# Kernel optimization log

Measured on AMD Instinct MI355X. Metric: run time of the kernel, lower is better.

## Reference

```python
import jax, jax.numpy as jnp
import numpy as np
import math

# Product of P Lorentz hyperboloids, each of dim D (time coord first), curvature c (K = 1/c).
N, P, D = 30000, 4, 64   # nodes, sub-manifolds, dim per sub-manifold
E = 480000               # edges (COO sparse adjacency)
C_IN, C_OUT = 1.0, 1.0
MIN_NORM = 1e-15
EPS = 1e-7
MAX_NORM = 1000.0


def _arcosh(x):
    return jnp.log(x + jnp.sqrt(jnp.maximum(x * x - 1.0, MIN_NORM)))


def proj(x, K):
    # project onto hyperboloid: recompute time coordinate from space coords
    y = x[..., 1:]
    t = jnp.sqrt(jnp.maximum(K + jnp.sum(y * y, -1, keepdims=True), EPS))
    return jnp.concatenate([t, y], -1)


def proj_tan0(u):
    # tangent space at origin: zero out the time coordinate
    return jnp.concatenate([jnp.zeros_like(u[..., :1]), u[..., 1:]], -1)


def proj_tan(u, x, K):
    ux = jnp.sum(x[..., 1:] * u[..., 1:], -1, keepdims=True)
    t = ux / jnp.maximum(x[..., :1], MIN_NORM)
    return jnp.concatenate([t, u[..., 1:]], -1)


def expmap0(u, K):
    sqrtK = K ** 0.5
    sp = u[..., 1:]
    n = jnp.maximum(jnp.linalg.norm(sp, axis=-1, keepdims=True), MIN_NORM)
    theta = n / sqrtK
    time = sqrtK * jnp.cosh(theta)
    space = sqrtK * jnp.sinh(theta) * sp / n
    return proj(jnp.concatenate([time, space], -1), K)


def logmap0(x, K):
    sqrtK = K ** 0.5
    sp = x[..., 1:]
    n = jnp.maximum(jnp.linalg.norm(sp, axis=-1, keepdims=True), MIN_NORM)
    theta = jnp.maximum(x[..., :1] / sqrtK, 1.0 + EPS)
    space = sqrtK * _arcosh(theta) * sp / n
    return jnp.concatenate([jnp.zeros_like(theta), space], -1)


def mink_dot(x, y):
    return jnp.sum(x[..., 1:] * y[..., 1:], -1, keepdims=True) - x[..., :1] * y[..., :1]


def expmap(u, x, K):
    sqrtK = K ** 0.5
    normu = jnp.minimum(jnp.sqrt(jnp.maximum(mink_dot(u, u), EPS)), MAX_NORM)
    theta = jnp.maximum(normu / sqrtK, MIN_NORM)
    return proj(jnp.cosh(theta) * x + jnp.sinh(theta) * u / theta, K)


def ptransp0(x, u, K):
    # parallel transport of tangent u at origin to point x
    sqrtK = K ** 0.5
    x0 = x[..., :1]
    y = x[..., 1:]
    yn = jnp.maximum(jnp.linalg.norm(y, axis=-1, keepdims=True), MIN_NORM)
    yu = y / yn
    v = jnp.concatenate([-yn, (sqrtK - x0) * yu], -1)
    alpha = jnp.sum(yu * u[..., 1:], -1, keepdims=True) / sqrtK
    return proj_tan(u - alpha * v, x, K)


def mobius_add(x, y, K):
    return expmap(ptransp0(x, logmap0(y, K), K), x, K)


def setup_inputs() -> dict:
    key = jax.random.key(0)
    k1, k2, k3, k4, k5 = jax.random.split(key, 5)
    K = 1.0 / C_IN
    # valid points on the product manifold: expmap0 of random tangent vectors
    t = 0.1 * jax.random.normal(k1, (N, P, D), dtype=jnp.float32)
    x = proj(expmap0(proj_tan0(t), K), K).reshape(N, P * D)
    adj_row = jax.random.randint(k2, (E,), 0, N)
    adj_col = jax.random.randint(k3, (E,), 0, N)
    # roughly degree-normalized positive adjacency weights
    adj_val = jax.random.uniform(k4, (E,), dtype=jnp.float32) / 16.0
    fan = P * D
    gain = math.sqrt(2.0) * math.sqrt(2.0 / (fan + fan))  # xavier_uniform(gain=sqrt(2)) scale
    weight = gain * jax.random.normal(k5, (fan, fan), dtype=jnp.float32)
    bias = jnp.full((fan,), 1e-4, dtype=jnp.float32)  # init.constant_(bias, 0.0001)
    return {"x": x, "adj_val": adj_val, "weight": weight, "bias": bias,
            "adj_row": adj_row, "adj_col": adj_col}


def reference(x, adj_val, weight, bias, adj_row, adj_col):
    K = 1.0 / C_IN
    Ko = 1.0 / C_OUT
    xs = x.reshape(N, P, D)

    # ---- ProLinear: mobius_matvec + hyperbolic bias add ----
    u = logmap0(xs, K).reshape(N, P * D)          # tangent at origin, concat across sub-manifolds
    mu = (u @ weight.T).reshape(N, P, D)          # [N, P*D] @ [P*D, P*D]^T
    h = proj(expmap0(proj_tan0(mu), K), K)
    b = bias.reshape(1, P, D)
    hyp_bias = proj(expmap0(proj_tan0(b), K), K)
    h = proj(mobius_add(h, hyp_bias, K), K)

    # ---- ProAgg: logmap0 -> spmm -> clamp -> expmap0 ----
    xt = logmap0(h, K).reshape(N, P * D)
    msgs = adj_val[:, None] * xt[adj_col]          # [E, P*D] gather
    support = jax.ops.segment_sum(msgs, adj_row, num_segments=N)
    support = jnp.minimum(support, MAX_NORM).reshape(N, P, D)
    h = proj(expmap0(proj_tan0(support), K), K)

    # ---- ProAct: logmap0 (c_in) -> clamped relu -> expmap0 (c_out) ----
    t = logmap0(h, K)
    t = jnp.minimum(jax.nn.relu(t), MAX_NORM)
    out = expmap0(proj_tan0(t), Ko)
    return out.reshape(N, P * D)
```

## Files before the change

### kernel.cpp

```cpp
#include <hip/hip_runtime.h>
#include <hip/hip_bf16.h>

#define MIN_NORM 1e-15f
#define EPS 1e-7f
#define MAX_NORM 1000.0f

#define NN 30000
#define PP 4
#define DD 64
#define EE 480000

typedef __attribute__((ext_vector_type(8))) short short8v;
typedef __attribute__((ext_vector_type(4))) float float4v;

__device__ inline float frcp(float x) { return __builtin_amdgcn_rcpf(x); }
__device__ inline float bf2f(unsigned short u) { return __uint_as_float(((unsigned)u) << 16); }
__device__ inline unsigned short f2bf(float f) {
    unsigned u = __float_as_uint(f);
    return (unsigned short)((u + 0x7fffu + ((u >> 16) & 1u)) >> 16);
}

__device__ inline float wsum(float v) {
#pragma unroll
    for (int off = 32; off >= 1; off >>= 1) v += __shfl_xor(v, off, 64);
    return v;
}
__device__ inline float expmap0_proj_pt(float v, int lane) {
    float sp = (lane == 0) ? 0.f : v;
    float n2 = wsum(sp * sp);
    float n = fmaxf(sqrtf(n2), MIN_NORM);
    float ep = __expf(n), em = frcp(ep);
    float s = 0.5f * (ep - em) * frcp(n);
    float time = sqrtf(fmaxf(1.f + s * s * n2, EPS));
    return (lane == 0) ? time : s * sp;
}
__device__ inline float logmap0_pt(float x, int lane) {
    float sp = (lane == 0) ? 0.f : x;
    float n2 = wsum(sp * sp);
    float n = fmaxf(sqrtf(n2), MIN_NORM);
    float x0 = __shfl(x, 0, 64);
    float th = fmaxf(x0, 1.f + EPS);
    float ac = __logf(th + sqrtf(fmaxf(th * th - 1.f, MIN_NORM)));
    return (lane == 0) ? 0.f : (ac * sp * frcp(n));
}
__device__ inline float gsum16(float v) {
#pragma unroll
    for (int off = 8; off >= 1; off >>= 1) v += __shfl_xor(v, off, 64);
    return v;
}
__device__ inline void gsum16x4(float& a, float& b, float& c, float& d) {
#pragma unroll
    for (int off = 8; off >= 1; off >>= 1) {
        a += __shfl_xor(a, off, 64);
        b += __shfl_xor(b, off, 64);
        c += __shfl_xor(c, off, 64);
        d += __shfl_xor(d, off, 64);
    }
}

__global__ void prep_kernel(const float* __restrict__ w,
                            unsigned short* __restrict__ bhi,
                            unsigned short* __restrict__ blo) {
    int tt = blockIdx.x * 256 + threadIdx.x;
    int lane = tt & 63;
    int ks = (tt >> 6) & 7;
    int nt = tt >> 9;
    int col = nt * 16 + (lane & 15);
    int kb = ks * 32 + (lane >> 4) * 8;
#pragma unroll
    for (int e = 0; e < 8; e++) {
        float v = w[col * 256 + kb + e];
        unsigned short h = f2bf(v);
        bhi[tt * 8 + e] = h;
        blo[tt * 8 + e] = f2bf(v - bf2f(h));
    }
}

#define GR 16
#define UPITCH 264
__global__ __launch_bounds__(256) void fused_front_hist_kernel(const float* __restrict__ x,
                                                               const unsigned short* __restrict__ bhi,
                                                               const unsigned short* __restrict__ blo,
                                                               const float* __restrict__ bias,
                                                               unsigned short* __restrict__ xt,
                                                               const int* __restrict__ adj_row,
                                                               int* __restrict__ counts) {
    __shared__ __align__(16) char smem[17952];
    unsigned short* uh = (unsigned short*)smem;
    unsigned short* ul = (unsigned short*)(smem + 8448);
    float* uspL = (float*)(smem + 16896);
    float* u2L  = (float*)(smem + 17920);

    int tid = threadIdx.x;
    int lane = tid & 63;
    int wv = tid >> 6;
    int row0 = blockIdx.x * GR;

    atomicAdd(&counts[adj_row[blockIdx.x * 256 + tid]], 1);

    {
        float b = bias[wv * 64 + lane];
        float y = expmap0_proj_pt(b, lane);
        float usp = logmap0_pt(y, lane);
        float U2 = wsum(usp * usp);
        uspL[wv * 64 + lane] = usp;
        if (lane == 0) u2L[wv] = U2;
    }

    int r = tid >> 4, l = tid & 15;
    {
        const float4* xr = (const float4*)(x + (size_t)(row0 + r) * 256);
        float4 a[4];
#pragma unroll
        for (int p = 0; p < 4; p++) a[p] = xr[p * 16 + l];
        float s0, s1, s2, s3;
        {
            float m0 = (l == 0) ? 0.f : a[0].x;
            float m1 = (l == 0) ? 0.f : a[1].x;
            float m2 = (l == 0) ? 0.f : a[2].x;
            float m3 = (l == 0) ? 0.f : a[3].x;
            s0 = m0 * m0 + a[0].y * a[0].y + a[0].z * a[0].z + a[0].w * a[0].w;
            s1 = m1 * m1 + a[1].y * a[1].y + a[1].z * a[1].z + a[1].w * a[1].w;
            s2 = m2 * m2 + a[2].y * a[2].y + a[2].z * a[2].z + a[2].w * a[2].w;
            s3 = m3 * m3 + a[3].y * a[3].y + a[3].z * a[3].z + a[3].w * a[3].w;
        }
        gsum16x4(s0, s1, s2, s3);
        float n2a[4] = {s0, s1, s2, s3};
#pragma unroll
        for (int p = 0; p < 4; p++) {
            float n2 = n2a[p];
            float n = fmaxf(sqrtf(n2), MIN_NORM);
            float th = fmaxf(sqrtf(1.f + n2), 1.f + EPS);
            float ac = __logf(th + sqrtf(fmaxf(th * th - 1.f, MIN_NORM)));
            float sc = ac * frcp(n);
            float ux0 = (l == 0) ? 0.f : sc * a[p].x;
            float uy = sc * a[p].y, uz = sc * a[p].z, uw = sc * a[p].w;
            unsigned short hx = f2bf(ux0), hy = f2bf(uy), hz = f2bf(uz), hw = f2bf(uw);
            ushort4 hv = {hx, hy, hz, hw};
            ushort4 lv = {f2bf(ux0 - bf2f(hx)), f2bf(uy - bf2f(hy)),
                          f2bf(uz - bf2f(hz)), f2bf(uw - bf2f(hw))};
            *(ushort4*)(uh + r * UPITCH + p * 64 + 4 * l) = hv;
            *(ushort4*)(ul + r * UPITCH + p * 64 + 4 * l) = lv;
        }
    }
    __syncthreads();

    float4v acc[4];
#pragma unroll
    for (int j = 0; j < 4; j++) acc[j] = (float4v){0.f, 0.f, 0.f, 0.f};
    int abyte = (lane & 15) * (UPITCH * 2) + (lane >> 4) * 16;
#pragma unroll
    for (int ks = 0; ks < 8; ks++) {
        short8v Ah = *(const short8v*)(smem + abyte + ks * 64);
        short8v Al = *(const short8v*)(smem + 8448 + abyte + ks * 64);
#pragma unroll
        for (int j = 0; j < 4; j++) {
            size_t chunk = ((size_t)((wv * 4 + j) * 8 + ks) * 64 + lane) * 8;
            short8v Bh = *(const short8v*)(bhi + chunk);
            short8v Bl = *(const short8v*)(blo + chunk);
            acc[j] = __builtin_amdgcn_mfma_f32_16x16x32_bf16(Ah, Bh, acc[j], 0, 0, 0);
            acc[j] = __builtin_amdgcn_mfma_f32_16x16x32_bf16(Al, Bh, acc[j], 0, 0, 0);
            acc[j] = __builtin_amdgcn_mfma_f32_16x16x32_bf16(Ah, Bl, acc[j], 0, 0, 0);
        }
    }

    int lp = lane & 15, hi = lane >> 4;
    float uf[4];
#pragma unroll
    for (int j = 0; j < 4; j++) uf[j] = uspL[wv * 64 + j * 16 + lp];
    if (lp == 0) {
        acc[0][0] = 0.f; acc[0][1] = 0.f; acc[0][2] = 0.f; acc[0][3] = 0.f;
    }
    float n2v[4], duv[4];
#pragma unroll
    for (int reg = 0; reg < 4; reg++) {
        float pn = 0.f, pd = 0.f;
#pragma unroll
        for (int j = 0; j < 4; j++) {
            pn = fmaf(acc[j][reg], acc[j][reg], pn);
            pd = fmaf(acc[j][reg], uf[j], pd);
        }
        n2v[reg] = pn; duv[reg] = pd;
    }
#pragma unroll
    for (int off = 1; off < 16; off <<= 1) {
#pragma unroll
        for (int reg = 0; reg < 4; reg++) {
            n2v[reg] += __shfl_xor(n2v[reg], off, 64);
            duv[reg] += __shfl_xor(duv[reg], off, 64);
        }
    }
    float U2 = u2L[wv];

    float A[4], Bc[4];
#pragma unroll
    for (int reg = 0; reg < 4; reg++) {
        float n2 = n2v[reg], duu = duv[reg];
        float n = fmaxf(sqrtf(n2), MIN_NORM);
        float epv = __expf(n), emv = frcp(epv);
        float sv = 0.5f * (epv - emv) * frcp(n);
        float hs2 = sv * sv * n2;
        float h0 = sqrtf(fmaxf(1.f + hs2, EPS));
        float yn = fmaxf(sv * n, MIN_NORM);
        float dhu = sv * duu;
        float alpha = dhu * frcp(yn);
        float g = alpha * (1.f - h0);
        float ux = dhu - g * yn;
        float t = ux * frcp(fmaxf(h0, MIN_NORM));
        float w2 = U2 - 2.f * g * alpha + g * g;
        float md = w2 - t * t;
        float normu = fminf(sqrtf(fmaxf(md, EPS)), MAX_NORM);
        float theta = fmaxf(normu, MIN_NORM);
        float ep2 = __expf(theta), em2 = frcp(ep2);
        float ch = 0.5f * (ep2 + em2);
        float shot = 0.5f * (ep2 - em2) * frcp(theta);
        float rn2 = ch * ch * hs2 + 2.f * ch * shot * ux + shot * shot * w2;
        float rtime = sqrtf(fmaxf(1.f + rn2, EPS));
        float th2 = fmaxf(rtime, 1.f + EPS);
        float ac2 = __logf(th2 + sqrtf(fmaxf(th2 * th2 - 1.f, MIN_NORM)));
        float rn = fmaxf(sqrtf(rn2), MIN_NORM);
        float K = ac2 * frcp(rn);
        A[reg] = K * sv * (ch - shot * g * frcp(yn));
        Bc[reg] = K * shot;
    }

    unsigned short* xbase = xt + (size_t)(row0 + hi * 4) * 256 + wv * 64 + lp;
#pragma unroll
    for (int reg = 0; reg < 4; reg++) {
#pragma unroll
        for (int j = 0; j < 4; j++) {
            float o = fmaf(A[reg], acc[j][reg], Bc[reg] * uf[j]);
            xbase[reg * 256 + j * 16] = f2bf(o);
        }
    }
}

#define SCH 32
__global__ __launch_bounds__(1024) void scan_kernel(const int* __restrict__ counts,
                                                    int* __restrict__ starts, int n) {
    int tid = threadIdx.x, lane = tid & 63, wv = tid >> 6;
    int i0 = tid * SCH;
    int c[SCH];
    const int4* c4 = (const int4*)(counts + i0);
#pragma unroll
    for (int q = 0; q < 8; q++) {
        int4 v = c4[q];
        c[4 * q] = v.x; c[4 * q + 1] = v.y; c[4 * q + 2] = v.z; c[4 * q + 3] = v.w;
    }
    int s = 0;
#pragma unroll
    for (int j = 0; j < SCH; j++) s += c[j];
    int incl = s;
#pragma unroll
    for (int off = 1; off < 64; off <<= 1) {
        int t = __shfl_up(incl, off, 64);
        if (lane >= off) incl += t;
    }
    __shared__ int wtot[16];
    if (lane == 63) wtot[wv] = incl;
    __syncthreads();
    if (wv == 0 && lane < 16) {
        int v = wtot[lane];
        int sc = v;
#pragma unroll
        for (int off = 1; off < 16; off <<= 1) {
            int t = __shfl_up(sc, off, 64);
            if (lane >= off) sc += t;
        }
        wtot[lane] = sc - v;
    }
    __syncthreads();
    int run = incl - s + wtot[wv];
#pragma unroll
    for (int j = 0; j < SCH; j++) {
        int idx = i0 + j;
        if (idx < n) starts[idx] = run;
        run += c[j];
    }
    if (tid == 1023) starts[n] = run;
}

__global__ void scatter_kernel(const int* __restrict__ row, const int* __restrict__ col,
                               const float* __restrict__ val, const int* __restrict__ starts,
                               int* __restrict__ cursor, int2* __restrict__ ep, int E) {
    int e = blockIdx.x * 256 + threadIdx.x;
    if (e < E) {
        int r = row[e];
        int pos = starts[r] + atomicAdd(&cursor[r], 1);
        ep[pos] = make_int2(col[e], __float_as_int(val[e]));
    }
}

__global__ __launch_bounds__(256) void spmm_final_kernel(const unsigned short* __restrict__ xt,
                                                         const int2* __restrict__ ep,
                                                         const int* __restrict__ starts,
                                                         float4* __restrict__ out4) {
    int w = threadIdx.x >> 6;
    int lane = threadIdx.x & 63;
    int r = blockIdx.x * 4 + w;
    int s = starts[r], e = starts[r + 1];

    float4 acc = {0.f, 0.f, 0.f, 0.f};
    for (int i = s; i < e; i += 8) {
        int cs[8]; float vs[8];
#pragma unroll
        for (int u = 0; u < 8; u++) {
            int idx = i + u;
            bool ok = idx < e;
            int2 pe = ep[ok ? idx : s];
            cs[u] = pe.x;
            vs[u] = ok ? __int_as_float(pe.y) : 0.f;
        }
        ushort4 av[8];
#pragma unroll
        for (int u = 0; u < 8; u++)
            av[u] = *(const ushort4*)(xt + ((size_t)cs[u] << 8) + (lane << 2));
#pragma unroll
        for (int u = 0; u < 8; u++) {
            acc.x = fmaf(vs[u], bf2f(av[u].x), acc.x);
            acc.y = fmaf(vs[u], bf2f(av[u].y), acc.y);
            acc.z = fmaf(vs[u], bf2f(av[u].z), acc.z);
            acc.w = fmaf(vs[u], bf2f(av[u].w), acc.w);
        }
    }

    acc.x = fminf(acc.x, MAX_NORM); acc.y = fminf(acc.y, MAX_NORM);
    acc.z = fminf(acc.z, MAX_NORM); acc.w = fminf(acc.w, MAX_NORM);

    bool leader = ((lane & 15) == 0);
    float4 sp = acc;
    if (leader) sp.x = 0.f;
    float n2 = gsum16(sp.x * sp.x + sp.y * sp.y + sp.z * sp.z + sp.w * sp.w);
    float n = fmaxf(sqrtf(n2), MIN_NORM);
    float ep1 = __expf(n), em1 = frcp(ep1);
    float s1 = 0.5f * (ep1 - em1) * frcp(n);
    float hs2 = s1 * s1 * n2;
    float time = sqrtf(fmaxf(1.f + hs2, EPS));
    float th = fmaxf(time, 1.f + EPS);
    float ac = __logf(th + sqrtf(fmaxf(th * th - 1.f, MIN_NORM)));
    float hn = fmaxf(s1 * n, MIN_NORM);
    float sc = ac * s1 * frcp(hn);
    float4 t;
    t.x = leader ? 0.f : sc * sp.x;
    t.y = sc * sp.y;
    t.z = sc * sp.z;
    t.w = sc * sp.w;
    t.x = fminf(fmaxf(t.x, 0.f), MAX_NORM);
    t.y = fminf(fmaxf(t.y, 0.f), MAX_NORM);
    t.z = fminf(fmaxf(t.z, 0.f), MAX_NORM);
    t.w = fminf(fmaxf(t.w, 0.f), MAX_NORM);
    float t2 = gsum16(t.x * t.x + t.y * t.y + t.z * t.z + t.w * t.w);
    float nt = fmaxf(sqrtf(t2), MIN_NORM);
    float ep3 = __expf(nt), em3 = frcp(ep3);
    float s3 = 0.5f * (ep3 - em3) * frcp(nt);
    float time3 = sqrtf(fmaxf(1.f + s3 * s3 * t2, EPS));
    float4 o;
    o.x = leader ? time3 : s3 * t.x;
    o.y = s3 * t.y;
    o.z = s3 * t.z;
    o.w = s3 * t.w;

    out4[(size_t)r * 64 + lane] = o;
}

extern "C" void kernel_launch(void* const* d_in, const int* in_sizes, int n_in,
                              void* d_out, int out_size, void* d_ws, size_t ws_size,
                              hipStream_t stream) {
    const float* x       = (const float*)d_in[0];
    const float* adj_val = (const float*)d_in[1];
    const float* weight  = (const float*)d_in[2];
    const float* bias    = (const float*)d_in[3];
    const int*   adj_row = (const int*)d_in[4];
    const int*   adj_col = (const int*)d_in[5];

    const int N = NN, E = EE;

    unsigned short* B   = (unsigned short*)d_ws;
    unsigned short* Whi = B + (size_t)N * 256;
    unsigned short* Wlo = Whi + 65536;
    int* counts  = (int*)(Wlo + 65536);
    int* cursor  = counts + N;
    int* starts  = cursor + N;
    int2* ep     = (int2*)(starts + N + 2);

    hipMemsetAsync(counts, 0, 2 * N * sizeof(int), stream);
    prep_kernel<<<32, 256, 0, stream>>>(weight, Whi, Wlo);
    fused_front_hist_kernel<<<N / GR, 256, 0, stream>>>(x, Whi, Wlo, bias, B,
                                                        adj_row, counts);
    scan_kernel<<<1, 1024, 0, stream>>>(counts, starts, N);
    scatter_kernel<<<(E + 255) / 256, 256, 0, stream>>>(adj_row, adj_col, adj_val,
                                                        starts, cursor, ep, E);
    spmm_final_kernel<<<N / 4, 256, 0, stream>>>(B, ep, starts, (float4*)d_out);
}
```

Measured before the change: 149.9 us.

## Hoist bias transform, dedupe per-row scalar math, packed bf16 cvt, dynamic row queue in spmm

The bias expmap/logmap computation moves out of every front block into one extra block of the prep kernel, and its results are read from global memory. Per-row scalar math in the front kernel (arcosh scale, A/B coefficients) is now computed once per lane and broadcast with shuffles instead of being repeated in every lane. The bf16 hi/lo split uses the packed v_cvt_pk_bf16_f32 instruction. The spmm kernel switches to a persistent grid of 2048 blocks in which each wavefront pulls rows from an atomic counter, to balance uneven row degrees. This adds atomic traffic and reads ep entries past a row's end, with column indices clamped and values zeroed.

```diff
diff --git a/kernel.cpp b/kernel.cpp
--- a/kernel.cpp
+++ b/kernel.cpp
@@ -18,6 +18,11 @@
 __device__ inline unsigned short f2bf(float f) {
     unsigned u = __float_as_uint(f);
     return (unsigned short)((u + 0x7fffu + ((u >> 16) & 1u)) >> 16);
+}
+__device__ inline unsigned pk_bf16(float a, float b) {
+    unsigned r;
+    asm("v_cvt_pk_bf16_f32 %0, %1, %2" : "=v"(r) : "v"(a), "v"(b));
+    return r;
 }
 
 __device__ inline float wsum(float v) {
@@ -60,7 +65,21 @@
 
 __global__ void prep_kernel(const float* __restrict__ w,
                             unsigned short* __restrict__ bhi,
-                            unsigned short* __restrict__ blo) {
+                            unsigned short* __restrict__ blo,
+                            const float* __restrict__ bias,
+                            float* __restrict__ uspG,
+                            float* __restrict__ u2G) {
+    if (blockIdx.x == 32) {
+        int lane = threadIdx.x & 63;
+        int wv = threadIdx.x >> 6;
+        float b = bias[wv * 64 + lane];
+        float y = expmap0_proj_pt(b, lane);
+        float usp = logmap0_pt(y, lane);
+        float U2 = wsum(usp * usp);
+        uspG[wv * 64 + lane] = usp;
+        if (lane == 0) u2G[wv] = U2;
+        return;
+    }
     int tt = blockIdx.x * 256 + threadIdx.x;
     int lane = tt & 63;
     int ks = (tt >> 6) & 7;
@@ -81,15 +100,14 @@
 __global__ __launch_bounds__(256) void fused_front_hist_kernel(const float* __restrict__ x,
                                                                const unsigned short* __restrict__ bhi,
                                                                const unsigned short* __restrict__ blo,
-                                                               const float* __restrict__ bias,
+                                                               const float* __restrict__ uspG,
+                                                               const float* __restrict__ u2G,
                                                                unsigned short* __restrict__ xt,
                                                                const int* __restrict__ adj_row,
                                                                int* __restrict__ counts) {
-    __shared__ __align__(16) char smem[17952];
+    __shared__ __align__(16) char smem[16896];
     unsigned short* uh = (unsigned short*)smem;
     unsigned short* ul = (unsigned short*)(smem + 8448);
-    float* uspL = (float*)(smem + 16896);
-    float* u2L  = (float*)(smem + 17920);
 
     int tid = threadIdx.x;
     int lane = tid & 63;
@@ -97,15 +115,6 @@
     int row0 = blockIdx.x * GR;
 
     atomicAdd(&counts[adj_row[blockIdx.x * 256 + tid]], 1);
-
-    {
-        float b = bias[wv * 64 + lane];
-        float y = expmap0_proj_pt(b, lane);
-        float usp = logmap0_pt(y, lane);
-        float U2 = wsum(usp * usp);
-        uspL[wv * 64 + lane] = usp;
-        if (lane == 0) u2L[wv] = U2;
-    }
 
     int r = tid >> 4, l = tid & 15;
     {
@@ -125,22 +134,28 @@
             s3 = m3 * m3 + a[3].y * a[3].y + a[3].z * a[3].z + a[3].w * a[3].w;
         }
         gsum16x4(s0, s1, s2, s3);
-        float n2a[4] = {s0, s1, s2, s3};
+        float n2m = (l & 2) ? ((l & 1) ? s3 : s2) : ((l & 1) ? s1 : s0);
+        float scm;
+        {
+            float n = fmaxf(sqrtf(n2m), MIN_NORM);
+            float th = fmaxf(sqrtf(1.f + n2m), 1.f + EPS);
+            float ac = __logf(th + sqrtf(fmaxf(th * th - 1.f, MIN_NORM)));
+            scm = ac * frcp(n);
+        }
+        int gbase = lane & 48;
 #pragma unroll
         for (int p = 0; p < 4; p++) {
-            float n2 = n2a[p];
-            float n = fmaxf(sqrtf(n2), MIN_NORM);
-            float th = fmaxf(sqrtf(1.f + n2), 1.f + EPS);
-            float ac = __logf(th + sqrtf(fmaxf(th * th - 1.f, MIN_NORM)));
-            float sc = ac * frcp(n);
-            float ux0 = (l == 0) ? 0.f : sc * a[p].x;
-            float uy = sc * a[p].y, uz = sc * a[p].z, uw = sc * a[p].w;
-            unsigned short hx = f2bf(ux0), hy = f2bf(uy), hz = f2bf(uz), hw = f2bf(uw);
-            ushort4 hv = {hx, hy, hz, hw};
-            ushort4 lv = {f2bf(ux0 - bf2f(hx)), f2bf(uy - bf2f(hy)),
-                          f2bf(uz - bf2f(hz)), f2bf(uw - bf2f(hw))};
-            *(ushort4*)(uh + r * UPITCH + p * 64 + 4 * l) = hv;
-            *(ushort4*)(ul + r * UPITCH + p * 64 + 4 * l) = lv;
+            float sc = __shfl(scm, gbase + p, 64);
+            float u0 = (l == 0) ? 0.f : sc * a[p].x;
+            float u1 = sc * a[p].y, u2 = sc * a[p].z, u3 = sc * a[p].w;
+            unsigned h01 = pk_bf16(u0, u1), h23 = pk_bf16(u2, u3);
+            float r0 = u0 - __uint_as_float(h01 << 16);
+            float r1 = u1 - __uint_as_float(h01 & 0xFFFF0000u);
+            float r2 = u2 - __uint_as_float(h23 << 16);
+            float r3 = u3 - __uint_as_float(h23 & 0xFFFF0000u);
+            unsigned lo01 = pk_bf16(r0, r1), lo23 = pk_bf16(r2, r3);
+            *(uint2*)(uh + r * UPITCH + p * 64 + 4 * l) = make_uint2(h01, h23);
+            *(uint2*)(ul + r * UPITCH + p * 64 + 4 * l) = make_uint2(lo01, lo23);
         }
     }
     __syncthreads();
@@ -167,7 +182,8 @@
     int lp = lane & 15, hi = lane >> 4;
     float uf[4];
 #pragma unroll
-    for (int j = 0; j < 4; j++) uf[j] = uspL[wv * 64 + j * 16 + lp];
+    for (int j = 0; j < 4; j++) uf[j] = uspG[wv * 64 + j * 16 + lp];
+    float U2 = u2G[wv];
     if (lp == 0) {
         acc[0][0] = 0.f; acc[0][1] = 0.f; acc[0][2] = 0.f; acc[0][3] = 0.f;
     }
@@ -190,12 +206,12 @@
             duv[reg] += __shfl_xor(duv[reg], off, 64);
         }
     }
-    float U2 = u2L[wv];
-
-    float A[4], Bc[4];
-#pragma unroll
-    for (int reg = 0; reg < 4; reg++) {
-        float n2 = n2v[reg], duu = duv[reg];
+
+    float Am, Bm;
+    {
+        int sel = lp & 3;
+        float n2 = (sel & 2) ? ((sel & 1) ? n2v[3] : n2v[2]) : ((sel & 1) ? n2v[1] : n2v[0]);
+        float duu = (sel & 2) ? ((sel & 1) ? duv[3] : duv[2]) : ((sel & 1) ? duv[1] : duv[0]);
         float n = fmaxf(sqrtf(n2), MIN_NORM);
         float epv = __expf(n), emv = frcp(epv);
         float sv = 0.5f * (epv - emv) * frcp(n);
@@ -220,16 +236,19 @@
         float ac2 = __logf(th2 + sqrtf(fmaxf(th2 * th2 - 1.f, MIN_NORM)));
         float rn = fmaxf(sqrtf(rn2), MIN_NORM);
         float K = ac2 * frcp(rn);
-        A[reg] = K * sv * (ch - shot * g * frcp(yn));
-        Bc[reg] = K * shot;
-    }
+        Am = K * sv * (ch - shot * g * frcp(yn));
+        Bm = K * shot;
+    }
+    int gbase = lane & 48;
 
     unsigned short* xbase = xt + (size_t)(row0 + hi * 4) * 256 + wv * 64 + lp;
 #pragma unroll
     for (int reg = 0; reg < 4; reg++) {
+        float A = __shfl(Am, gbase + reg, 64);
+        float B = __shfl(Bm, gbase + reg, 64);
 #pragma unroll
         for (int j = 0; j < 4; j++) {
-            float o = fmaf(A[reg], acc[j][reg], Bc[reg] * uf[j]);
+            float o = fmaf(A, acc[j][reg], B * uf[j]);
             xbase[reg * 256 + j * 16] = f2bf(o);
         }
     }
@@ -294,73 +313,75 @@
 __global__ __launch_bounds__(256) void spmm_final_kernel(const unsigned short* __restrict__ xt,
                                                          const int2* __restrict__ ep,
                                                          const int* __restrict__ starts,
+                                                         int* __restrict__ qctr,
                                                          float4* __restrict__ out4) {
-    int w = threadIdx.x >> 6;
     int lane = threadIdx.x & 63;
-    int r = blockIdx.x * 4 + w;
-    int s = starts[r], e = starts[r + 1];
-
-    float4 acc = {0.f, 0.f, 0.f, 0.f};
-    for (int i = s; i < e; i += 8) {
-        int cs[8]; float vs[8];
-#pragma unroll
-        for (int u = 0; u < 8; u++) {
-            int idx = i + u;
-            bool ok = idx < e;
-            int2 pe = ep[ok ? idx : s];
-            cs[u] = pe.x;
-            vs[u] = ok ? __int_as_float(pe.y) : 0.f;
-        }
-        ushort4 av[8];
-#pragma unroll
-        for (int u = 0; u < 8; u++)
-            av[u] = *(const ushort4*)(xt + ((size_t)cs[u] << 8) + (lane << 2));
-#pragma unroll
-        for (int u = 0; u < 8; u++) {
-            acc.x = fmaf(vs[u], bf2f(av[u].x), acc.x);
-            acc.y = fmaf(vs[u], bf2f(av[u].y), acc.y);
-            acc.z = fmaf(vs[u], bf2f(av[u].z), acc.z);
-            acc.w = fmaf(vs[u], bf2f(av[u].w), acc.w);
-        }
-    }
-
-    acc.x = fminf(acc.x, MAX_NORM); acc.y = fminf(acc.y, MAX_NORM);
-    acc.z = fminf(acc.z, MAX_NORM); acc.w = fminf(acc.w, MAX_NORM);
-
-    bool leader = ((lane & 15) == 0);
-    float4 sp = acc;
-    if (leader) sp.x = 0.f;
-    float n2 = gsum16(sp.x * sp.x + sp.y * sp.y + sp.z * sp.z + sp.w * sp.w);
-    float n = fmaxf(sqrtf(n2), MIN_NORM);
-    float ep1 = __expf(n), em1 = frcp(ep1);
-    float s1 = 0.5f * (ep1 - em1) * frcp(n);
-    float hs2 = s1 * s1 * n2;
-    float time = sqrtf(fmaxf(1.f + hs2, EPS));
-    float th = fmaxf(time, 1.f + EPS);
-    float ac = __logf(th + sqrtf(fmaxf(th * th - 1.f, MIN_NORM)));
-    float hn = fmaxf(s1 * n, MIN_NORM);
-    float sc = ac * s1 * frcp(hn);
-    float4 t;
-    t.x = leader ? 0.f : sc * sp.x;
-    t.y = sc * sp.y;
-    t.z = sc * sp.z;
-    t.w = sc * sp.w;
-    t.x = fminf(fmaxf(t.x, 0.f), MAX_NORM);
-    t.y = fminf(fmaxf(t.y, 0.f), MAX_NORM);
-    t.z = fminf(fmaxf(t.z, 0.f), MAX_NORM);
-    t.w = fminf(fmaxf(t.w, 0.f), MAX_NORM);
-    float t2 = gsum16(t.x * t.x + t.y * t.y + t.z * t.z + t.w * t.w);
-    float nt = fmaxf(sqrtf(t2), MIN_NORM);
-    float ep3 = __expf(nt), em3 = frcp(ep3);
-    float s3 = 0.5f * (ep3 - em3) * frcp(nt);
-    float time3 = sqrtf(fmaxf(1.f + s3 * s3 * t2, EPS));
-    float4 o;
-    o.x = leader ? time3 : s3 * t.x;
-    o.y = s3 * t.y;
-    o.z = s3 * t.z;
-    o.w = s3 * t.w;
-
-    out4[(size_t)r * 64 + lane] = o;
+    for (;;) {
+        int r0 = 0;
+        if (lane == 0) r0 = atomicAdd(qctr, 1);
+        int r = __shfl(r0, 0, 64);
+        if (r >= NN) return;
+        int s = starts[r], e = starts[r + 1];
+
+        float4 acc = {0.f, 0.f, 0.f, 0.f};
+        for (int i = s; i < e; i += 8) {
+            int2 pe[8];
+#pragma unroll
+            for (int u = 0; u < 8; u++) pe[u] = ep[i + u];
+            ushort4 av[8]; float vs[8];
+#pragma unroll
+            for (int u = 0; u < 8; u++) {
+                int c = min(max(pe[u].x, 0), NN - 1);
+                vs[u] = (i + u < e) ? __int_as_float(pe[u].y) : 0.f;
+                av[u] = *(const ushort4*)(xt + ((size_t)c << 8) + (lane << 2));
+            }
+#pragma unroll
+            for (int u = 0; u < 8; u++) {
+                acc.x = fmaf(vs[u], bf2f(av[u].x), acc.x);
+                acc.y = fmaf(vs[u], bf2f(av[u].y), acc.y);
+                acc.z = fmaf(vs[u], bf2f(av[u].z), acc.z);
+                acc.w = fmaf(vs[u], bf2f(av[u].w), acc.w);
+            }
+        }
+
+        acc.x = fminf(acc.x, MAX_NORM); acc.y = fminf(acc.y, MAX_NORM);
+        acc.z = fminf(acc.z, MAX_NORM); acc.w = fminf(acc.w, MAX_NORM);
+
+        bool leader = ((lane & 15) == 0);
+        float4 sp = acc;
+        if (leader) sp.x = 0.f;
+        float n2 = gsum16(sp.x * sp.x + sp.y * sp.y + sp.z * sp.z + sp.w * sp.w);
+        float n = fmaxf(sqrtf(n2), MIN_NORM);
+        float ep1 = __expf(n), em1 = frcp(ep1);
+        float s1 = 0.5f * (ep1 - em1) * frcp(n);
+        float hs2 = s1 * s1 * n2;
+        float time = sqrtf(fmaxf(1.f + hs2, EPS));
+        float th = fmaxf(time, 1.f + EPS);
+        float ac = __logf(th + sqrtf(fmaxf(th * th - 1.f, MIN_NORM)));
+        float hn = fmaxf(s1 * n, MIN_NORM);
+        float sc = ac * s1 * frcp(hn);
+        float4 t;
+        t.x = leader ? 0.f : sc * sp.x;
+        t.y = sc * sp.y;
+        t.z = sc * sp.z;
+        t.w = sc * sp.w;
+        t.x = fminf(fmaxf(t.x, 0.f), MAX_NORM);
+        t.y = fminf(fmaxf(t.y, 0.f), MAX_NORM);
+        t.z = fminf(fmaxf(t.z, 0.f), MAX_NORM);
+        t.w = fminf(fmaxf(t.w, 0.f), MAX_NORM);
+        float t2 = gsum16(t.x * t.x + t.y * t.y + t.z * t.z + t.w * t.w);
+        float nt = fmaxf(sqrtf(t2), MIN_NORM);
+        float ep3 = __expf(nt), em3 = frcp(ep3);
+        float s3 = 0.5f * (ep3 - em3) * frcp(nt);
+        float time3 = sqrtf(fmaxf(1.f + s3 * s3 * t2, EPS));
+        float4 o;
+        o.x = leader ? time3 : s3 * t.x;
+        o.y = s3 * t.y;
+        o.z = s3 * t.z;
+        o.w = s3 * t.w;
+
+        out4[(size_t)r * 64 + lane] = o;
+    }
 }
 
 extern "C" void kernel_launch(void* const* d_in, const int* in_sizes, int n_in,
@@ -378,17 +399,20 @@
     unsigned short* B   = (unsigned short*)d_ws;
     unsigned short* Whi = B + (size_t)N * 256;
     unsigned short* Wlo = Whi + 65536;
-    int* counts  = (int*)(Wlo + 65536);
+    float* uspG  = (float*)(Wlo + 65536);
+    float* u2G   = uspG + 256;
+    int* counts  = (int*)(u2G + 8);
     int* cursor  = counts + N;
-    int* starts  = cursor + N;
+    int* qctr    = cursor + N;
+    int* starts  = qctr + 2;
     int2* ep     = (int2*)(starts + N + 2);
 
-    hipMemsetAsync(counts, 0, 2 * N * sizeof(int), stream);
-    prep_kernel<<<32, 256, 0, stream>>>(weight, Whi, Wlo);
-    fused_front_hist_kernel<<<N / GR, 256, 0, stream>>>(x, Whi, Wlo, bias, B,
+    hipMemsetAsync(counts, 0, (2 * N + 2) * sizeof(int), stream);
+    prep_kernel<<<33, 256, 0, stream>>>(weight, Whi, Wlo, bias, uspG, u2G);
+    fused_front_hist_kernel<<<N / GR, 256, 0, stream>>>(x, Whi, Wlo, uspG, u2G, B,
                                                         adj_row, counts);
     scan_kernel<<<1, 1024, 0, stream>>>(counts, starts, N);
     scatter_kernel<<<(E + 255) / 256, 256, 0, stream>>>(adj_row, adj_col, adj_val,
                                                         starts, cursor, ep, E);
-    spmm_final_kernel<<<N / 4, 256, 0, stream>>>(B, ep, starts, (float4*)d_out);
-}
+    spmm_final_kernel<<<2048, 256, 0, stream>>>(B, ep, starts, qctr, (float4*)d_out);
+}
```

Measured after the change: 550.9 us. 268% more time.
